# Kernel tuning notes

Hardware: AMD Instinct MI355X
Metric: run time of the kernel (lower is better)

The kernel has to match this reference:

```python
import jax, jax.numpy as jnp
import numpy as np

B, S, HID = 2, 2048, 1024
H, KVH, D = 16, 4, 64
N_REP = H // KVH
SCALE = D ** -0.5
CAP = 50.0


def rotate_half(x):
    x1, x2 = x[..., : D // 2], x[..., D // 2 :]
    return jnp.concatenate((-x2, x1), axis=-1)


def setup_inputs() -> dict:
    key = jax.random.key(0)
    ks = jax.random.split(key, 10)
    X = jax.random.normal(ks[0], (B, S, HID), dtype=jnp.float32)
    # RoPE tables: (B, S, D)
    inv_freq = 1.0 / (10000.0 ** (np.arange(0, D, 2, dtype=np.float32) / D))
    pos = np.arange(S, dtype=np.float32)
    freqs = np.outer(pos, inv_freq)  # (S, D/2)
    emb = np.concatenate([freqs, freqs], axis=-1)  # (S, D)
    cos = jnp.broadcast_to(jnp.asarray(np.cos(emb)), (B, S, D))
    sin = jnp.broadcast_to(jnp.asarray(np.sin(emb)), (B, S, D))
    # causal mask: 1 where key <= query
    mask = jnp.broadcast_to(jnp.tril(jnp.ones((S, S), dtype=jnp.int32)), (B, S, S))
    std = HID ** -0.5
    Wq = jax.random.normal(ks[1], (HID, HID), dtype=jnp.float32) * std
    bq = jnp.zeros((HID,), dtype=jnp.float32)
    Wk = jax.random.normal(ks[2], (KVH * D, HID), dtype=jnp.float32) * std
    bk = jnp.zeros((KVH * D,), dtype=jnp.float32)
    Wv = jax.random.normal(ks[3], (KVH * D, HID), dtype=jnp.float32) * std
    bv = jnp.zeros((KVH * D,), dtype=jnp.float32)
    Wo = jax.random.normal(ks[4], (HID, HID), dtype=jnp.float32) * std
    bo = jnp.zeros((HID,), dtype=jnp.float32)
    return {"X": X, "cos": cos, "sin": sin, "mask": mask,
            "Wq": Wq, "bq": bq, "Wk": Wk, "bk": bk,
            "Wv": Wv, "bv": bv, "Wo": Wo, "bo": bo}


def reference(X, cos, sin, mask, Wq, bq, Wk, bk, Wv, bv, Wo, bo):
    bsz, q_len, _ = X.shape
    q = (X @ Wq.T + bq).reshape(bsz, q_len, H, D).transpose(0, 2, 1, 3)    # (B,H,S,D)
    k = (X @ Wk.T + bk).reshape(bsz, q_len, KVH, D).transpose(0, 2, 1, 3)  # (B,KVH,S,D)
    v = (X @ Wv.T + bv).reshape(bsz, q_len, KVH, D).transpose(0, 2, 1, 3)
    c = cos[:, None, :, :]  # (B,1,S,D)
    s = sin[:, None, :, :]
    q = q * c + rotate_half(q) * s
    k = k * c + rotate_half(k) * s
    k = jnp.repeat(k, N_REP, axis=1)  # GQA expand -> (B,H,S,D)
    v = jnp.repeat(v, N_REP, axis=1)
    scores = jnp.einsum('bhqd,bhkd->bhqk', q, k) * SCALE
    scores = jnp.clip(scores, -CAP, CAP)  # attention cap
    scores = jnp.where(mask[:, None, :, :] == 0, -1e9, scores)
    attn = jax.nn.softmax(scores, axis=-1)  # dropout p=0 -> identity
    ctx = jnp.einsum('bhqk,bhkd->bhqd', attn, v)
    ctx = ctx.transpose(0, 2, 1, 3).reshape(bsz, q_len, H * D)
    out = ctx @ Wo.T + bo
    return (out, attn)
```

## Files before the change

kernel.cpp:

```cpp
#include <hip/hip_runtime.h>
#include <cstdint>
#include <cstddef>

#define S_LEN   2048
#define BATCH   2
#define HID_DIM 1024
#define NHEAD   16
#define NKV     4
#define DHEAD   64
#define SCALE_F 0.125f
#define L2E     1.44269504f
#define QSCALE  (SCALE_F * L2E)
#define CAPL2   (50.0f * L2E)

typedef unsigned short u16;
typedef __attribute__((ext_vector_type(8))) short  short8_t;
typedef __attribute__((ext_vector_type(4))) float  f32x4;
typedef __attribute__((ext_vector_type(4))) u16    u16x4;

static __device__ __forceinline__ u16 f2bf(float f) {
  uint32_t x = __builtin_bit_cast(uint32_t, f);
  x += 0x7fffu + ((x >> 16) & 1u);
  return (u16)(x >> 16);
}

static __device__ __forceinline__ void gload_lds16(const void* g, void* l) {
  __builtin_amdgcn_global_load_lds((const __attribute__((address_space(1))) void*)g,
                                   (__attribute__((address_space(3))) void*)l, 16, 0, 0);
}

static __device__ __forceinline__ float exp2med3(float x) {
  return __builtin_amdgcn_exp2f(__builtin_amdgcn_fmed3f(x, -CAPL2, CAPL2));
}

__global__ void cast_all(const float* __restrict__ X,  u16* __restrict__ xb,
                         const float* __restrict__ Wq, u16* __restrict__ wqb,
                         const float* __restrict__ Wk, u16* __restrict__ wkb,
                         const float* __restrict__ Wv, u16* __restrict__ wvb,
                         const float* __restrict__ Wo, u16* __restrict__ wob) {
  const float* src; u16* dst; int n4;
  switch (blockIdx.y) {
    case 0:  src = X;  dst = xb;  n4 = (BATCH * S_LEN * HID_DIM) / 4; break;
    case 1:  src = Wq; dst = wqb; n4 = (HID_DIM * HID_DIM) / 4;       break;
    case 2:  src = Wk; dst = wkb; n4 = (NKV * DHEAD * HID_DIM) / 4;   break;
    case 3:  src = Wv; dst = wvb; n4 = (NKV * DHEAD * HID_DIM) / 4;   break;
    default: src = Wo; dst = wob; n4 = (HID_DIM * HID_DIM) / 4;       break;
  }
  for (int i = blockIdx.x * 256 + threadIdx.x; i < n4; i += gridDim.x * 256) {
    f32x4 v = ((const f32x4*)src)[i];
    u16x4 o;
    o[0] = f2bf(v[0]); o[1] = f2bf(v[1]); o[2] = f2bf(v[2]); o[3] = f2bf(v[3]);
    ((u16x4*)dst)[i] = o;
  }
}

__global__ __launch_bounds__(256, 4) void gemm_qkv(const u16* __restrict__ Xb,
                                                   const u16* __restrict__ Wqb,
                                                   const u16* __restrict__ Wkb,
                                                   const u16* __restrict__ Wvb,
                                                   const float* __restrict__ bq,
                                                   const float* __restrict__ bk,
                                                   const float* __restrict__ bv,
                                                   const float* __restrict__ cosb,
                                                   const float* __restrict__ sinb,
                                                   u16* __restrict__ qout,
                                                   u16* __restrict__ kout,
                                                   u16* __restrict__ vtout) {
  __shared__ u16 As[64 * 64];
  __shared__ u16 Bs[128 * 64];
  const int tid = threadIdx.x, lane = tid & 63, wid = tid >> 6;
  const int l15 = lane & 15, lg = lane >> 4;
  const int m0 = blockIdx.x * 64, n0 = blockIdx.y * 128;
  const int wm = wid & 1, wn = wid >> 1;
  const int K = HID_DIM;

  const u16* Wp; const float* biasp; int nl, mode;
  if (n0 < 1024)      { Wp = Wqb; biasp = bq; nl = n0;        mode = 0; }
  else if (n0 < 1280) { Wp = Wkb; biasp = bk; nl = n0 - 1024; mode = 1; }
  else                { Wp = Wvb; biasp = bv; nl = n0 - 1280; mode = 2; }

  f32x4 acc[4][2];
  #pragma unroll
  for (int a = 0; a < 4; ++a)
    #pragma unroll
    for (int b2 = 0; b2 < 2; ++b2) acc[a][b2] = (f32x4){0.f, 0.f, 0.f, 0.f};

  const int srow = (lane >> 3), sg = (lane & 7);

  for (int kk = 0; kk < K; kk += 64) {
    __syncthreads();
    #pragma unroll
    for (int i = 0; i < 6; ++i) {
      const int c = wid * 6 + i;
      if (c < 8) {
        const int r = c * 8 + srow;
        const int g = sg ^ (r & 7);
        gload_lds16(Xb + (size_t)(m0 + r) * K + kk + g * 8, As + c * 512);
      } else {
        const int cb = c - 8;
        const int r = cb * 8 + srow;
        const int g = sg ^ (r & 7);
        gload_lds16(Wp + (size_t)(nl + r) * K + kk + g * 8, Bs + cb * 512);
      }
    }
    __syncthreads();
    #pragma unroll
    for (int ks = 0; ks < 2; ++ks) {
      short8_t xa[2], wb[4];
      #pragma unroll
      for (int f = 0; f < 2; ++f) {
        const int rm = wm * 32 + f * 16 + l15;
        xa[f] = *(const short8_t*)(As + rm * 64 + (((ks * 4 + lg) ^ (rm & 7)) * 8));
      }
      #pragma unroll
      for (int f = 0; f < 4; ++f) {
        const int rn = wn * 64 + f * 16 + l15;
        wb[f] = *(const short8_t*)(Bs + rn * 64 + (((ks * 4 + lg) ^ (rn & 7)) * 8));
      }
      if (mode != 2) {
        #pragma unroll
        for (int fn = 0; fn < 4; ++fn)
          #pragma unroll
          for (int fm = 0; fm < 2; ++fm)
            acc[fn][fm] = __builtin_amdgcn_mfma_f32_16x16x32_bf16(wb[fn], xa[fm], acc[fn][fm], 0, 0, 0);
      } else {
        #pragma unroll
        for (int fn = 0; fn < 4; ++fn)
          #pragma unroll
          for (int fm = 0; fm < 2; ++fm)
            acc[fn][fm] = __builtin_amdgcn_mfma_f32_16x16x32_bf16(xa[fm], wb[fn], acc[fn][fm], 0, 0, 0);
      }
    }
  }

  const int m_base = m0 + wm * 32;
  const int nlb = nl + wn * 64;

  if (mode < 2) {
    const int Nout = (mode == 0) ? HID_DIM : (NKV * DHEAD);
    const float qs = (mode == 0) ? QSCALE : 1.0f;
    u16* outb = (mode == 0) ? qout : kout;
    #pragma unroll
    for (int fm = 0; fm < 2; ++fm) {
      const int row = m_base + fm * 16 + l15;
      #pragma unroll
      for (int fn = 0; fn < 2; ++fn) {
        const int dh = fn * 16 + lg * 4;
        const f32x4 c4 = *(const f32x4*)(cosb + (size_t)row * 64 + dh);
        const f32x4 s4 = *(const f32x4*)(sinb + (size_t)row * 64 + dh);
        f32x4 x1 = acc[fn][fm]     + *(const f32x4*)(biasp + nlb + fn * 16 + lg * 4);
        f32x4 x2 = acc[fn + 2][fm] + *(const f32x4*)(biasp + nlb + (fn + 2) * 16 + lg * 4);
        f32x4 o1 = (x1 * c4 - x2 * s4) * qs;
        f32x4 o2 = (x2 * c4 + x1 * s4) * qs;
        u16x4 u1, u2;
        #pragma unroll
        for (int i = 0; i < 4; ++i) { u1[i] = f2bf(o1[i]); u2[i] = f2bf(o2[i]); }
        *(u16x4*)(outb + (size_t)row * Nout + nlb + fn * 16 + lg * 4)       = u1;
        *(u16x4*)(outb + (size_t)row * Nout + nlb + (fn + 2) * 16 + lg * 4) = u2;
      }
    }
  } else {
    #pragma unroll
    for (int fn = 0; fn < 4; ++fn) {
      const int d = nlb + fn * 16 + l15;
      const float bvs = biasp[d];
      #pragma unroll
      for (int fm = 0; fm < 2; ++fm) {
        const int s0 = m_base + fm * 16 + lg * 4;
        const int b_ = s0 >> 11, s_ = s0 & (S_LEN - 1);
        u16x4 o;
        #pragma unroll
        for (int i = 0; i < 4; ++i) o[i] = f2bf(acc[fn][fm][i] + bvs);
        *(u16x4*)(vtout + (size_t)(b_ * 256 + d) * S_LEN + s_) = o;
      }
    }
  }
}

__global__ __launch_bounds__(256, 4) void gemm_out(const u16* __restrict__ A,
                                                   const u16* __restrict__ W,
                                                   const float* __restrict__ bias,
                                                   float* __restrict__ outp) {
  __shared__ u16 As[64 * 64];
  __shared__ u16 Bs[128 * 64];
  const int tid = threadIdx.x, lane = tid & 63, wid = tid >> 6;
  const int l15 = lane & 15, lg = lane >> 4;
  const int m0 = blockIdx.x * 64, n0 = blockIdx.y * 128;
  const int wm = wid & 1, wn = wid >> 1;
  const int K = HID_DIM, N = HID_DIM;

  f32x4 acc[4][2];
  #pragma unroll
  for (int a = 0; a < 4; ++a)
    #pragma unroll
    for (int b2 = 0; b2 < 2; ++b2) acc[a][b2] = (f32x4){0.f, 0.f, 0.f, 0.f};

  const int srow = (lane >> 3), sg = (lane & 7);

  for (int kk = 0; kk < K; kk += 64) {
    __syncthreads();
    #pragma unroll
    for (int i = 0; i < 6; ++i) {
      const int c = wid * 6 + i;
      if (c < 8) {
        const int r = c * 8 + srow;
        const int g = sg ^ (r & 7);
        gload_lds16(A + (size_t)(m0 + r) * K + kk + g * 8, As + c * 512);
      } else {
        const int cb = c - 8;
        const int r = cb * 8 + srow;
        const int g = sg ^ (r & 7);
        gload_lds16(W + (size_t)(n0 + r) * K + kk + g * 8, Bs + cb * 512);
      }
    }
    __syncthreads();
    #pragma unroll
    for (int ks = 0; ks < 2; ++ks) {
      short8_t xa[2], wb[4];
      #pragma unroll
      for (int f = 0; f < 2; ++f) {
        const int rm = wm * 32 + f * 16 + l15;
        xa[f] = *(const short8_t*)(As + rm * 64 + (((ks * 4 + lg) ^ (rm & 7)) * 8));
      }
      #pragma unroll
      for (int f = 0; f < 4; ++f) {
        const int rn = wn * 64 + f * 16 + l15;
        wb[f] = *(const short8_t*)(Bs + rn * 64 + (((ks * 4 + lg) ^ (rn & 7)) * 8));
      }
      #pragma unroll
      for (int fn = 0; fn < 4; ++fn)
        #pragma unroll
        for (int fm = 0; fm < 2; ++fm)
          acc[fn][fm] = __builtin_amdgcn_mfma_f32_16x16x32_bf16(wb[fn], xa[fm], acc[fn][fm], 0, 0, 0);
    }
  }

  const int m_base = m0 + wm * 32, n_base = n0 + wn * 64;
  #pragma unroll
  for (int fn = 0; fn < 4; ++fn) {
    const int col = n_base + fn * 16 + lg * 4;
    const f32x4 bvv = *(const f32x4*)(bias + col);
    #pragma unroll
    for (int fm = 0; fm < 2; ++fm) {
      const int row = m_base + fm * 16 + l15;
      *(f32x4*)(outp + (size_t)row * N + col) = acc[fn][fm] + bvv;
    }
  }
}

__global__ __launch_bounds__(256, 4) void attn_fused(const u16* __restrict__ qb,
                                                     const u16* __restrict__ kb,
                                                     const u16* __restrict__ vtb,
                                                     float* __restrict__ attn,
                                                     u16* __restrict__ ctxb) {
  __shared__ u16 kS[2][64 * 64];
  __shared__ u16 vS[64 * 64];
  __shared__ u16 pS[4][16][72];

  const int tid = threadIdx.x, lane = tid & 63, wid = tid >> 6;
  const int l15 = lane & 15, lg = lane >> 4;
  const int bh = blockIdx.x, b = bh >> 4, h = bh & 15, kvh = h >> 2;
  const int qt = (int)(gridDim.y - 1 - blockIdx.y);
  const int q0 = qt * 64;
  const int NT = qt + 1;
  const int qw = q0 + wid * 16;
  const int qrow = qw + l15;

  const u16* qp = qb + (size_t)(b * S_LEN + qrow) * HID_DIM + h * DHEAD + lg * 8;
  const short8_t qf0 = *(const short8_t*)qp;
  const short8_t qf1 = *(const short8_t*)(qp + 32);

  const u16* kbase  = kb  + (size_t)(b * S_LEN) * (NKV * DHEAD) + kvh * DHEAD;
  const u16* vtbase = vtb + (size_t)(b * NKV + kvh) * DHEAD * S_LEN;

  const int sr8 = wid * 8 + (lane >> 3);
  const int sgr = lane & 7;

  auto stageK = [&](int bi, int kv0) {
    #pragma unroll
    for (int it = 0; it < 2; ++it) {
      const int r = it * 32 + sr8;
      const int g = sgr ^ (r & 7);
      gload_lds16(kbase + (size_t)(kv0 + r) * (NKV * DHEAD) + g * 8,
                  &kS[bi][(it * 32 + wid * 8) * 64]);
    }
  };
  auto stageV = [&](int kv0) {
    #pragma unroll
    for (int it = 0; it < 2; ++it) {
      const int r = it * 32 + sr8;
      const int g = sgr ^ (r & 7);
      gload_lds16(vtbase + (size_t)r * S_LEN + kv0 + g * 8,
                  &vS[(it * 32 + wid * 8) * 64]);
    }
  };

  f32x4 lacc = (f32x4){0.f, 0.f, 0.f, 0.f};
  stageK(0, 0);
  for (int t = 0; t < NT; ++t) {
    const int kv0 = t * 64;
    if (t + 1 < NT) {
      stageK((t + 1) & 1, kv0 + 64);
      asm volatile("s_waitcnt vmcnt(2)" ::: "memory");
    } else {
      asm volatile("s_waitcnt vmcnt(0)" ::: "memory");
    }
    __builtin_amdgcn_s_barrier();
    const u16* ks = kS[t & 1];
    const bool maskc = (kv0 + 63 > qw);
    #pragma unroll
    for (int g16 = 0; g16 < 4; ++g16) {
      const int r = g16 * 16 + l15;
      short8_t ka0 = *(const short8_t*)(ks + r * 64 + ((lg ^ (r & 7)) * 8));
      short8_t ka1 = *(const short8_t*)(ks + r * 64 + (((4 + lg) ^ (r & 7)) * 8));
      f32x4 sacc = (f32x4){0.f, 0.f, 0.f, 0.f};
      sacc = __builtin_amdgcn_mfma_f32_16x16x32_bf16(ka0, qf0, sacc, 0, 0, 0);
      sacc = __builtin_amdgcn_mfma_f32_16x16x32_bf16(ka1, qf1, sacc, 0, 0, 0);
      #pragma unroll
      for (int i = 0; i < 4; ++i) {
        float e = exp2med3(sacc[i]);
        if (maskc) {
          const int kvi = kv0 + g16 * 16 + lg * 4 + i;
          e = (kvi <= qrow) ? e : 0.f;
        }
        lacc[i] += e;
      }
    }
    __builtin_amdgcn_s_barrier();
  }
  float lsum = (lacc[0] + lacc[1]) + (lacc[2] + lacc[3]);
  lsum += __shfl_xor(lsum, 16);
  lsum += __shfl_xor(lsum, 32);
  const float invl = 1.f / lsum;

  float* abase = attn + (size_t)bh * S_LEN * S_LEN;
  float* arow  = abase + (size_t)qrow * S_LEN;
  f32x4 ctx[4];
  #pragma unroll
  for (int dt = 0; dt < 4; ++dt) ctx[dt] = (f32x4){0.f, 0.f, 0.f, 0.f};

  stageK(0, 0);
  asm volatile("s_waitcnt vmcnt(0)" ::: "memory");
  __builtin_amdgcn_s_barrier();

  for (int t = 0; t < NT; ++t) {
    const int kv0 = t * 64;
    stageV(kv0);
    const bool pre = (t + 1 < NT);
    if (pre) stageK((t + 1) & 1, kv0 + 64);

    const u16* ks = kS[t & 1];
    const bool maskc = (kv0 + 63 > qw);
    #pragma unroll
    for (int g16 = 0; g16 < 4; ++g16) {
      const int r = g16 * 16 + l15;
      short8_t ka0 = *(const short8_t*)(ks + r * 64 + ((lg ^ (r & 7)) * 8));
      short8_t ka1 = *(const short8_t*)(ks + r * 64 + (((4 + lg) ^ (r & 7)) * 8));
      f32x4 sacc = (f32x4){0.f, 0.f, 0.f, 0.f};
      sacc = __builtin_amdgcn_mfma_f32_16x16x32_bf16(ka0, qf0, sacc, 0, 0, 0);
      sacc = __builtin_amdgcn_mfma_f32_16x16x32_bf16(ka1, qf1, sacc, 0, 0, 0);
      f32x4 pv; u16x4 pb;
      #pragma unroll
      for (int i = 0; i < 4; ++i) {
        float p = exp2med3(sacc[i]) * invl;
        if (maskc) {
          const int kvi = kv0 + g16 * 16 + lg * 4 + i;
          p = (kvi <= qrow) ? p : 0.f;
        }
        pv[i] = p;
        pb[i] = f2bf(p);
      }
      *(f32x4*)(arow + kv0 + g16 * 16 + lg * 4) = pv;
      *(u16x4*)&pS[wid][l15][g16 * 16 + lg * 4] = pb;
    }

    if (pre) asm volatile("s_waitcnt vmcnt(6)" ::: "memory");
    else     asm volatile("s_waitcnt vmcnt(4)" ::: "memory");
    __builtin_amdgcn_s_barrier();

    short8_t pa0 = *(const short8_t*)&pS[wid][l15][lg * 8];
    short8_t pa1 = *(const short8_t*)&pS[wid][l15][32 + lg * 8];
    #pragma unroll
    for (int dt = 0; dt < 4; ++dt) {
      const int r = dt * 16 + l15;
      short8_t bv0 = *(const short8_t*)(vS + r * 64 + ((lg ^ (r & 7)) * 8));
      short8_t bv1 = *(const short8_t*)(vS + r * 64 + (((4 + lg) ^ (r & 7)) * 8));
      ctx[dt] = __builtin_amdgcn_mfma_f32_16x16x32_bf16(bv0, pa0, ctx[dt], 0, 0, 0);
      ctx[dt] = __builtin_amdgcn_mfma_f32_16x16x32_bf16(bv1, pa1, ctx[dt], 0, 0, 0);
    }

    if (pre) {
      asm volatile("s_waitcnt vmcnt(4)" ::: "memory");
      __builtin_amdgcn_s_barrier();
    }
  }

  #pragma unroll
  for (int dt = 0; dt < 4; ++dt) {
    u16x4 o;
    #pragma unroll
    for (int i = 0; i < 4; ++i) o[i] = f2bf(ctx[dt][i]);
    *(u16x4*)(ctxb + (size_t)(b * S_LEN + qrow) * HID_DIM + h * DHEAD + dt * 16 + lg * 4) = o;
  }

  const int zc0 = q0 + 64;
  if (zc0 < S_LEN) {
    const f32x4 z = (f32x4){0.f, 0.f, 0.f, 0.f};
    for (int r = wid; r < 64; r += 4) {
      float* rowp = abase + (size_t)(q0 + r) * S_LEN;
      for (int c = zc0 + lane * 4; c < S_LEN; c += 256)
        *(f32x4*)(rowp + c) = z;
    }
  }
}

extern "C" void kernel_launch(void* const* d_in, const int* in_sizes, int n_in,
                              void* d_out, int out_size, void* d_ws, size_t ws_size,
                              hipStream_t stream) {
  (void)in_sizes; (void)n_in; (void)out_size; (void)ws_size;
  const float* X    = (const float*)d_in[0];
  const float* cosb = (const float*)d_in[1];
  const float* sinb = (const float*)d_in[2];
  const float* Wq = (const float*)d_in[4];
  const float* bq = (const float*)d_in[5];
  const float* Wk = (const float*)d_in[6];
  const float* bk = (const float*)d_in[7];
  const float* Wv = (const float*)d_in[8];
  const float* bv = (const float*)d_in[9];
  const float* Wo = (const float*)d_in[10];
  const float* bo = (const float*)d_in[11];

  float* outp  = (float*)d_out;
  float* attnp = outp + (size_t)BATCH * S_LEN * HID_DIM;

  const int M = BATCH * S_LEN;
  u16* ws    = (u16*)d_ws;
  u16* Xb    = ws;
  u16* Wqb   = Xb  + (size_t)M * HID_DIM;
  u16* Wkb   = Wqb + (size_t)HID_DIM * HID_DIM;
  u16* Wvb   = Wkb + (size_t)NKV * DHEAD * HID_DIM;
  u16* Wob   = Wvb + (size_t)NKV * DHEAD * HID_DIM;
  u16* qbuf  = Wob + (size_t)HID_DIM * HID_DIM;
  u16* kbuf  = qbuf + (size_t)M * HID_DIM;
  u16* vtbuf = kbuf + (size_t)M * NKV * DHEAD;
  u16* ctxb  = vtbuf + (size_t)M * NKV * DHEAD;

  cast_all<<<dim3(1024, 5), 256, 0, stream>>>(X, Xb, Wq, Wqb, Wk, Wkb, Wv, Wvb, Wo, Wob);

  gemm_qkv<<<dim3(M / 64, 12), 256, 0, stream>>>(Xb, Wqb, Wkb, Wvb, bq, bk, bv,
                                                 cosb, sinb, qbuf, kbuf, vtbuf);

  attn_fused<<<dim3(BATCH * NHEAD, S_LEN / 64), 256, 0, stream>>>(qbuf, kbuf, vtbuf, attnp, ctxb);

  gemm_out<<<dim3(M / 64, HID_DIM / 128), 256, 0, stream>>>(ctxb, Wob, bo, outp);
}
```

Baseline: 212.7 us.

## Split attention into row-sum/zero-fill kernel and separate PV kernel

```diff
diff --git a/kernel.cpp b/kernel.cpp
--- a/kernel.cpp
+++ b/kernel.cpp
@@ -248,30 +248,44 @@
   }
 }
 
-__global__ __launch_bounds__(256, 4) void attn_fused(const u16* __restrict__ qb,
-                                                     const u16* __restrict__ kb,
-                                                     const u16* __restrict__ vtb,
-                                                     float* __restrict__ attn,
-                                                     u16* __restrict__ ctxb) {
+__global__ __launch_bounds__(256, 6) void zl_kernel(const u16* __restrict__ qb,
+                                                    const u16* __restrict__ kb,
+                                                    float* __restrict__ invlp,
+                                                    float* __restrict__ attn) {
   __shared__ u16 kS[2][64 * 64];
-  __shared__ u16 vS[64 * 64];
-  __shared__ u16 pS[4][16][72];
-
+
+  const int idx = blockIdx.x;
+  const int unit = idx >> 1;
+  const int bh = unit & 31;
+  const int b = bh >> 4, h = bh & 15, kvh = h >> 2;
+  const int ut = unit >> 5;
   const int tid = threadIdx.x, lane = tid & 63, wid = tid >> 6;
+
+  if (idx & 1) {
+    const int q0 = ut * 64;
+    const int zc0 = q0 + 64;
+    if (zc0 >= S_LEN) return;
+    float* abase = attn + (size_t)bh * S_LEN * S_LEN;
+    const f32x4 z = (f32x4){0.f, 0.f, 0.f, 0.f};
+    for (int r = wid; r < 64; r += 4) {
+      float* rowp = abase + (size_t)(q0 + r) * S_LEN;
+      for (int c = zc0 + lane * 4; c < S_LEN; c += 256)
+        *(f32x4*)(rowp + c) = z;
+    }
+    return;
+  }
+
   const int l15 = lane & 15, lg = lane >> 4;
-  const int bh = blockIdx.x, b = bh >> 4, h = bh & 15, kvh = h >> 2;
-  const int qt = (int)(gridDim.y - 1 - blockIdx.y);
-  const int q0 = qt * 64;
+  const int qt = 31 - ut;
   const int NT = qt + 1;
-  const int qw = q0 + wid * 16;
+  const int qw = qt * 64 + wid * 16;
   const int qrow = qw + l15;
 
   const u16* qp = qb + (size_t)(b * S_LEN + qrow) * HID_DIM + h * DHEAD + lg * 8;
   const short8_t qf0 = *(const short8_t*)qp;
   const short8_t qf1 = *(const short8_t*)(qp + 32);
 
-  const u16* kbase  = kb  + (size_t)(b * S_LEN) * (NKV * DHEAD) + kvh * DHEAD;
-  const u16* vtbase = vtb + (size_t)(b * NKV + kvh) * DHEAD * S_LEN;
+  const u16* kbase = kb + (size_t)(b * S_LEN) * (NKV * DHEAD) + kvh * DHEAD;
 
   const int sr8 = wid * 8 + (lane >> 3);
   const int sgr = lane & 7;
@@ -283,15 +297,6 @@
       const int g = sgr ^ (r & 7);
       gload_lds16(kbase + (size_t)(kv0 + r) * (NKV * DHEAD) + g * 8,
                   &kS[bi][(it * 32 + wid * 8) * 64]);
-    }
-  };
-  auto stageV = [&](int kv0) {
-    #pragma unroll
-    for (int it = 0; it < 2; ++it) {
-      const int r = it * 32 + sr8;
-      const int g = sgr ^ (r & 7);
-      gload_lds16(vtbase + (size_t)r * S_LEN + kv0 + g * 8,
-                  &vS[(it * 32 + wid * 8) * 64]);
     }
   };
 
@@ -331,10 +336,59 @@
   float lsum = (lacc[0] + lacc[1]) + (lacc[2] + lacc[3]);
   lsum += __shfl_xor(lsum, 16);
   lsum += __shfl_xor(lsum, 32);
-  const float invl = 1.f / lsum;
-
-  float* abase = attn + (size_t)bh * S_LEN * S_LEN;
-  float* arow  = abase + (size_t)qrow * S_LEN;
+  if (lg == 0)
+    invlp[(size_t)bh * S_LEN + qrow] = 1.f / lsum;
+}
+
+__global__ __launch_bounds__(256, 4) void attn_pv(const u16* __restrict__ qb,
+                                                  const u16* __restrict__ kb,
+                                                  const u16* __restrict__ vtb,
+                                                  const float* __restrict__ invlp,
+                                                  float* __restrict__ attn,
+                                                  u16* __restrict__ ctxb) {
+  __shared__ u16 kS[2][64 * 64];
+  __shared__ u16 vS[64 * 64];
+  __shared__ u16 pS[4][16][72];
+
+  const int tid = threadIdx.x, lane = tid & 63, wid = tid >> 6;
+  const int l15 = lane & 15, lg = lane >> 4;
+  const int bh = blockIdx.x, b = bh >> 4, h = bh & 15, kvh = h >> 2;
+  const int qt = (int)(gridDim.y - 1 - blockIdx.y);
+  const int NT = qt + 1;
+  const int qw = qt * 64 + wid * 16;
+  const int qrow = qw + l15;
+
+  const u16* qp = qb + (size_t)(b * S_LEN + qrow) * HID_DIM + h * DHEAD + lg * 8;
+  const short8_t qf0 = *(const short8_t*)qp;
+  const short8_t qf1 = *(const short8_t*)(qp + 32);
+  const float invl = invlp[(size_t)bh * S_LEN + qrow];
+
+  const u16* kbase  = kb  + (size_t)(b * S_LEN) * (NKV * DHEAD) + kvh * DHEAD;
+  const u16* vtbase = vtb + (size_t)(b * NKV + kvh) * DHEAD * S_LEN;
+
+  const int sr8 = wid * 8 + (lane >> 3);
+  const int sgr = lane & 7;
+
+  auto stageK = [&](int bi, int kv0) {
+    #pragma unroll
+    for (int it = 0; it < 2; ++it) {
+      const int r = it * 32 + sr8;
+      const int g = sgr ^ (r & 7);
+      gload_lds16(kbase + (size_t)(kv0 + r) * (NKV * DHEAD) + g * 8,
+                  &kS[bi][(it * 32 + wid * 8) * 64]);
+    }
+  };
+  auto stageV = [&](int kv0) {
+    #pragma unroll
+    for (int it = 0; it < 2; ++it) {
+      const int r = it * 32 + sr8;
+      const int g = sgr ^ (r & 7);
+      gload_lds16(vtbase + (size_t)r * S_LEN + kv0 + g * 8,
+                  &vS[(it * 32 + wid * 8) * 64]);
+    }
+  };
+
+  float* arow = attn + (size_t)bh * S_LEN * S_LEN + (size_t)qrow * S_LEN;
   f32x4 ctx[4];
   #pragma unroll
   for (int dt = 0; dt < 4; ++dt) ctx[dt] = (f32x4){0.f, 0.f, 0.f, 0.f};
@@ -401,16 +455,6 @@
     #pragma unroll
     for (int i = 0; i < 4; ++i) o[i] = f2bf(ctx[dt][i]);
     *(u16x4*)(ctxb + (size_t)(b * S_LEN + qrow) * HID_DIM + h * DHEAD + dt * 16 + lg * 4) = o;
-  }
-
-  const int zc0 = q0 + 64;
-  if (zc0 < S_LEN) {
-    const f32x4 z = (f32x4){0.f, 0.f, 0.f, 0.f};
-    for (int r = wid; r < 64; r += 4) {
-      float* rowp = abase + (size_t)(q0 + r) * S_LEN;
-      for (int c = zc0 + lane * 4; c < S_LEN; c += 256)
-        *(f32x4*)(rowp + c) = z;
-    }
   }
 }
 
@@ -444,13 +488,17 @@
   u16* kbuf  = qbuf + (size_t)M * HID_DIM;
   u16* vtbuf = kbuf + (size_t)M * NKV * DHEAD;
   u16* ctxb  = vtbuf + (size_t)M * NKV * DHEAD;
+  float* invlp = (float*)(ctxb + (size_t)M * HID_DIM);
 
   cast_all<<<dim3(1024, 5), 256, 0, stream>>>(X, Xb, Wq, Wqb, Wk, Wkb, Wv, Wvb, Wo, Wob);
 
   gemm_qkv<<<dim3(M / 64, 12), 256, 0, stream>>>(Xb, Wqb, Wkb, Wvb, bq, bk, bv,
                                                  cosb, sinb, qbuf, kbuf, vtbuf);
 
-  attn_fused<<<dim3(BATCH * NHEAD, S_LEN / 64), 256, 0, stream>>>(qbuf, kbuf, vtbuf, attnp, ctxb);
+  zl_kernel<<<dim3(2048), 256, 0, stream>>>(qbuf, kbuf, invlp, attnp);
+
+  attn_pv<<<dim3(BATCH * NHEAD, S_LEN / 64), 256, 0, stream>>>(qbuf, kbuf, vtbuf,
+                                                               invlp, attnp, ctxb);
 
   gemm_out<<<dim3(M / 64, HID_DIM / 128), 256, 0, stream>>>(ctxb, Wob, bo, outp);
 }
```

New measurement: 234.8 us. +10.4%, slower.

## Stage attention probabilities through swizzled LDS to coalesce fp32 attn stores

Applied to the files above, without the earlier changes.

```diff
diff --git a/kernel.cpp b/kernel.cpp
--- a/kernel.cpp
+++ b/kernel.cpp
@@ -22,6 +22,9 @@
   uint32_t x = __builtin_bit_cast(uint32_t, f);
   x += 0x7fffu + ((x >> 16) & 1u);
   return (u16)(x >> 16);
+}
+static __device__ __forceinline__ float bf2f(u16 u) {
+  return __builtin_bit_cast(float, (uint32_t)u << 16);
 }
 
 static __device__ __forceinline__ void gload_lds16(const void* g, void* l) {
@@ -248,14 +251,14 @@
   }
 }
 
-__global__ __launch_bounds__(256, 4) void attn_fused(const u16* __restrict__ qb,
+__global__ __launch_bounds__(256, 5) void attn_fused(const u16* __restrict__ qb,
                                                      const u16* __restrict__ kb,
                                                      const u16* __restrict__ vtb,
                                                      float* __restrict__ attn,
                                                      u16* __restrict__ ctxb) {
   __shared__ u16 kS[2][64 * 64];
   __shared__ u16 vS[64 * 64];
-  __shared__ u16 pS[4][16][72];
+  __shared__ u16 pB[4][16][64];
 
   const int tid = threadIdx.x, lane = tid & 63, wid = tid >> 6;
   const int l15 = lane & 15, lg = lane >> 4;
@@ -334,10 +337,11 @@
   const float invl = 1.f / lsum;
 
   float* abase = attn + (size_t)bh * S_LEN * S_LEN;
-  float* arow  = abase + (size_t)qrow * S_LEN;
   f32x4 ctx[4];
   #pragma unroll
   for (int dt = 0; dt < 4; ++dt) ctx[dt] = (f32x4){0.f, 0.f, 0.f, 0.f};
+
+  const int r2 = lane >> 4, c16 = lane & 15;
 
   stageK(0, 0);
   asm volatile("s_waitcnt vmcnt(0)" ::: "memory");
@@ -359,7 +363,7 @@
       f32x4 sacc = (f32x4){0.f, 0.f, 0.f, 0.f};
       sacc = __builtin_amdgcn_mfma_f32_16x16x32_bf16(ka0, qf0, sacc, 0, 0, 0);
       sacc = __builtin_amdgcn_mfma_f32_16x16x32_bf16(ka1, qf1, sacc, 0, 0, 0);
-      f32x4 pv; u16x4 pb;
+      u16x4 pb;
       #pragma unroll
       for (int i = 0; i < 4; ++i) {
         float p = exp2med3(sacc[i]) * invl;
@@ -367,19 +371,35 @@
           const int kvi = kv0 + g16 * 16 + lg * 4 + i;
           p = (kvi <= qrow) ? p : 0.f;
         }
-        pv[i] = p;
         pb[i] = f2bf(p);
       }
-      *(f32x4*)(arow + kv0 + g16 * 16 + lg * 4) = pv;
-      *(u16x4*)&pS[wid][l15][g16 * 16 + lg * 4] = pb;
+      *(u16x4*)&pB[wid][l15][((g16 * 4 + lg) ^ l15) * 4] = pb;
+    }
+
+    #pragma unroll
+    for (int j = 0; j < 4; ++j) {
+      const int R = j * 4 + r2;
+      u16x4 pv4 = *(const u16x4*)&pB[wid][R][(c16 ^ R) * 4];
+      f32x4 v;
+      #pragma unroll
+      for (int i = 0; i < 4; ++i) v[i] = bf2f(pv4[i]);
+      *(f32x4*)(abase + (size_t)(qw + R) * S_LEN + kv0 + c16 * 4) = v;
     }
 
     if (pre) asm volatile("s_waitcnt vmcnt(6)" ::: "memory");
     else     asm volatile("s_waitcnt vmcnt(4)" ::: "memory");
     __builtin_amdgcn_s_barrier();
 
-    short8_t pa0 = *(const short8_t*)&pS[wid][l15][lg * 8];
-    short8_t pa1 = *(const short8_t*)&pS[wid][l15][32 + lg * 8];
+    u16x4 a0 = *(const u16x4*)&pB[wid][l15][((2 * lg) ^ l15) * 4];
+    u16x4 a1 = *(const u16x4*)&pB[wid][l15][((2 * lg + 1) ^ l15) * 4];
+    u16x4 b0 = *(const u16x4*)&pB[wid][l15][((8 + 2 * lg) ^ l15) * 4];
+    u16x4 b1 = *(const u16x4*)&pB[wid][l15][((9 + 2 * lg) ^ l15) * 4];
+    short8_t pa0, pa1;
+    #pragma unroll
+    for (int i = 0; i < 4; ++i) {
+      pa0[i] = (short)a0[i]; pa0[i + 4] = (short)a1[i];
+      pa1[i] = (short)b0[i]; pa1[i + 4] = (short)b1[i];
+    }
     #pragma unroll
     for (int dt = 0; dt < 4; ++dt) {
       const int r = dt * 16 + l15;
```

Result: faster. 205.7 us (-3.3%).
